# Performance work log

Hardware: AMD Instinct MI355X
Metric: run time of the kernel (lower is better)

The kernel has to match this reference:

```python
import jax, jax.numpy as jnp
import numpy as np

NFEATS = 768; NHIDS = 768; H = 8; HD = NHIDS // H
NT = 32768; NC = 32768; NS = 32768; DEG = 8; E = NT * DEG
ALPHA = 0.2  # LeakyReLU negative slope


def setup_inputs() -> dict:
    key = jax.random.key(0)
    ks = jax.random.split(key, 16)
    f32 = jnp.float32
    dst = jnp.repeat(jnp.arange(NT, dtype=jnp.int32), DEG)  # uniform in-degree mailbox
    return {
        'h': jax.random.normal(ks[0], (NT, NFEATS), f32),
        'hb_c_src': jax.random.normal(ks[1], (NC, NHIDS), f32),
        'hb_s_src': jax.random.normal(ks[2], (NS, NHIDS), f32),
        'Wg': jax.random.normal(ks[3], (H, NFEATS, HD), f32) * 0.05,
        'bg': jnp.zeros((H, HD), f32),
        'ag': jax.random.normal(ks[4], (H, 2 * HD), f32) * 0.1,
        'agb': jnp.zeros((H,), f32),
        'Wx': jax.random.normal(ks[5], (H, NHIDS, HD), f32) * 0.05,
        'bx': jnp.zeros((H, HD), f32),
        'ax': jax.random.normal(ks[6], (H, 2 * HD), f32) * 0.1,
        'axb': jnp.zeros((H,), f32),
        'Wih': jax.random.normal(ks[7], (3 * NHIDS, NHIDS), f32) * 0.02,
        'Whh': jax.random.normal(ks[8], (3 * NHIDS, NHIDS), f32) * 0.02,
        'bih': jnp.zeros((3 * NHIDS,), f32),
        'bhh': jnp.zeros((3 * NHIDS,), f32),
        'intra_src': jax.random.randint(ks[9], (E,), 0, NT, jnp.int32),
        'intra_dst': dst,
        'c_src': jax.random.randint(ks[10], (E,), 0, NC, jnp.int32),
        'c_dst': dst,
        's_src': jax.random.randint(ks[11], (E,), 0, NS, jnp.int32),
        's_dst': dst,
    }


def _attend(Wh_s, Wh_d, src, dst, a, ab, n_dst):
    """Multi-head GAT edge attention + segment softmax + weighted aggregation.
    Wh_s: [Ns,H,D] src projections, Wh_d: [Nd,H,D] dst projections.
    a([Wh_src||Wh_dst]) decomposed as a_src.Wh_src + a_dst.Wh_dst + bias."""
    D = Wh_s.shape[-1]
    e = (jnp.einsum('nhd,hd->nh', Wh_s, a[:, :D])[src]
         + jnp.einsum('nhd,hd->nh', Wh_d, a[:, D:])[dst] + ab)  # [E,H]
    e = jax.nn.leaky_relu(e, ALPHA)
    m = jax.ops.segment_max(e, dst, num_segments=n_dst)
    ex = jnp.exp(e - m[dst])
    den = jax.ops.segment_sum(ex, dst, num_segments=n_dst)
    att = ex / den[dst]  # per-dst softmax over incoming edges (DGL mailbox softmax)
    out = jax.ops.segment_sum(Wh_s[src] * att[..., None], dst, num_segments=n_dst)
    return out.reshape(n_dst, H * D)  # concat heads


def _forward(h, hb_c_src, hb_s_src, Wg, bg, ag, agb, Wx, bx, ax, axb,
             Wih, Whh, bih, bhh, intra_src, intra_dst, c_src, c_dst, s_src, s_dst):
    n = h.shape[0]
    # intra-turn GAT (x = self.gat(g, t)); dropout is identity in eval mode
    Wh = jnp.einsum('nf,hfd->nhd', h, Wg) + bg
    x = _attend(Wh, Wh, intra_src, intra_dst, ag, agb, n)
    # cross-turn inversed GAT; dst nodes' 'hb' feature is the fresh gat output x;
    # counter_bw and support_bw share the same xgat weights.
    Wx_d = jnp.einsum('nf,hfd->nhd', x, Wx) + bx
    Wc_s = jnp.einsum('nf,hfd->nhd', hb_c_src, Wx) + bx
    h_c = _attend(Wc_s, Wx_d, c_src, c_dst, ax, axb, n)
    Ws_s = jnp.einsum('nf,hfd->nhd', hb_s_src, Wx) + bx
    h_s = _attend(Ws_s, Wx_d, s_src, s_dst, ax, axb, n)
    hid = 0.5 * h_c + 0.5 * h_s
    # GRUCell(x, hid)
    gi = x @ Wih.T + bih
    gh = hid @ Whh.T + bhh
    ir, iz, inn = jnp.split(gi, 3, axis=1)
    hr, hz, hn = jnp.split(gh, 3, axis=1)
    r = jax.nn.sigmoid(ir + hr)
    z = jax.nn.sigmoid(iz + hz)
    cand = jnp.tanh(inn + r * hn)
    return (1.0 - z) * cand + z * hid


def reference(h, hb_c_src, hb_s_src, Wg, bg, ag, agb, Wx, bx, ax, axb,
              Wih, Whh, bih, bhh, intra_src, intra_dst, c_src, c_dst, s_src, s_dst):
    return _forward(h, hb_c_src, hb_s_src, Wg, bg, ag, agb, Wx, bx, ax, axb,
                    Wih, Whh, bih, bhh, intra_src, intra_dst, c_src, c_dst, s_src, s_dst)
```

## Files before the change

kernel.cpp:

```cpp
#include <hip/hip_runtime.h>
#include <hip/hip_bf16.h>
#include <math.h>

#define NT 32768
#define HD 96
#define DEG 8
#define NE (NT * DEG)
#define LRELU_ALPHA 0.2f
#define CH 16384

typedef __attribute__((ext_vector_type(8))) short bf16x8;
typedef __attribute__((ext_vector_type(8))) unsigned short u16x8;
typedef __attribute__((ext_vector_type(4))) unsigned short u16x4;
typedef __attribute__((ext_vector_type(4))) float f32x4;

__device__ __forceinline__ unsigned short f2bf(float x) {
    union { float f; unsigned u; } v; v.f = x;
    unsigned r = v.u + 0x7FFFu + ((v.u >> 16) & 1u);
    return (unsigned short)(r >> 16);
}
__device__ __forceinline__ float bf2f(unsigned short u) {
    union { unsigned u; float f; } v; v.u = ((unsigned)u) << 16; return v.f;
}

__device__ __forceinline__ void gload_lds16(const void* g, void* l) {
    __builtin_amdgcn_global_load_lds(
        (const __attribute__((address_space(1))) void*)g,
        (__attribute__((address_space(3))) void*)l, 16, 0, 0);
}


__global__ void packWT(const float* __restrict__ W, unsigned short* __restrict__ T) {
    int idx = blockIdx.x * 256 + threadIdx.x;
    if (idx >= 768 * 768) return;
    int c = idx / 768, f = idx % 768;
    T[idx] = f2bf(W[(size_t)(c / HD) * 768 * HD + (size_t)f * HD + (c % HD)]);
}

__global__ void cvt_bf8(const float* __restrict__ X, unsigned short* __restrict__ Y, int n8) {
    int i = blockIdx.x * 256 + threadIdx.x;
    if (i >= n8) return;
    float4 a = ((const float4*)X)[2 * i];
    float4 b = ((const float4*)X)[2 * i + 1];
    u16x8 p;
    p[0] = f2bf(a.x); p[1] = f2bf(a.y); p[2] = f2bf(a.z); p[3] = f2bf(a.w);
    p[4] = f2bf(b.x); p[5] = f2bf(b.y); p[6] = f2bf(b.z); p[7] = f2bf(b.w);
    ((u16x8*)Y)[i] = p;
}

__global__ void packWV(const float* __restrict__ Wx, const float* __restrict__ ax,
                       const float* __restrict__ bx,
                       float* __restrict__ wv, float* __restrict__ cd) {
    int idx = blockIdx.x * 256 + threadIdx.x;
    if (idx < 8 * 768) {
        int h = idx / 768, f = idx % 768;
        const float* wp = Wx + (size_t)h * 768 * HD + (size_t)f * HD;
        const float* ap = ax + h * 2 * HD + HD;
        float s = 0.f;
        for (int d = 0; d < HD; d++) s += wp[d] * ap[d];
        wv[idx] = s;
    }
    if (idx < 8) {
        const float* bp = bx + idx * HD;
        const float* ap = ax + idx * 2 * HD + HD;
        float s = 0.f;
        for (int d = 0; d < HD; d++) s += bp[d] * ap[d];
        cd[idx] = s;
    }
}

__global__ __launch_bounds__(256, 4) void mgemm3s(
    const float* __restrict__ A1, const float* __restrict__ A2,
    const float* __restrict__ A3,
    const unsigned short* __restrict__ BT1, const unsigned short* __restrict__ BT2,
    const float* __restrict__ bias1, const float* __restrict__ bias2,
    unsigned short* __restrict__ C1, unsigned short* __restrict__ C2,
    unsigned short* __restrict__ C3,
    int mt1, int mt2, int N, int K) {
    __shared__ unsigned short Alds[2][128 * 40];
    __shared__ unsigned short Blds[2][128 * 32];
    const int tid = threadIdx.x;
    const int w = tid >> 6, l = tid & 63;
    const int wr = w >> 1, wc = w & 1;
    const int lrow = l & 15, lk = l >> 4;

    const int nx = gridDim.x;
    const int nwg = nx * gridDim.y;
    int lin = blockIdx.y * nx + blockIdx.x;
    if ((nwg & 7) == 0) lin = (lin & 7) * (nwg >> 3) + (lin >> 3);
    int bm = lin / nx;
    const int bn = lin % nx;

    const int part = (bm >= mt1) + (bm >= mt2);
    const float* A           = part == 0 ? A1 : (part == 1 ? A2 : A3);
    const unsigned short* BT = part == 0 ? BT1 : BT2;
    const float* bias        = part == 0 ? bias1 : bias2;
    unsigned short* C        = part == 0 ? C1 : (part == 1 ? C2 : C3);
    bm -= (part == 1 ? mt1 : (part == 2 ? mt2 : 0));

    const unsigned short* bsrc[2];
    #pragma unroll
    for (int q = 0; q < 2; q++) {
        int idx = q * 256 + tid;
        int r = idx >> 2, s = idx & 3;
        int kw = s ^ ((r >> 1) & 3);
        bsrc[q] = BT + (size_t)(bn * 128 + r) * K + kw * 8;
    }
    const int ldst = (w * 64) * 8;

    const int arow = tid >> 1;
    const int as0 = (tid & 1) * 2;
    const float* aptr = A + (size_t)(bm * 128 + arow) * K + as0 * 8;

    auto stageA = [&](int buf, int k0) {
        float4 a0 = *(const float4*)(aptr + k0);
        float4 a1 = *(const float4*)(aptr + k0 + 4);
        float4 a2 = *(const float4*)(aptr + k0 + 8);
        float4 a3 = *(const float4*)(aptr + k0 + 12);
        u16x8 p0, p1;
        p0[0] = f2bf(a0.x); p0[1] = f2bf(a0.y); p0[2] = f2bf(a0.z); p0[3] = f2bf(a0.w);
        p0[4] = f2bf(a1.x); p0[5] = f2bf(a1.y); p0[6] = f2bf(a1.z); p0[7] = f2bf(a1.w);
        p1[0] = f2bf(a2.x); p1[1] = f2bf(a2.y); p1[2] = f2bf(a2.z); p1[3] = f2bf(a2.w);
        p1[4] = f2bf(a3.x); p1[5] = f2bf(a3.y); p1[6] = f2bf(a3.z); p1[7] = f2bf(a3.w);
        *(u16x8*)(&Alds[buf][arow * 40 + as0 * 8]) = p0;
        *(u16x8*)(&Alds[buf][arow * 40 + as0 * 8 + 8]) = p1;
    };

    gload_lds16(bsrc[0], &Blds[0][ldst]);
    gload_lds16(bsrc[1], &Blds[0][2048 + ldst]);
    stageA(0, 0);

    f32x4 acc[4][4] = {};
    const int nt = K >> 5;

    for (int t = 0; t < nt; ++t) {
        const int cur = t & 1;
        __syncthreads();
        if (t + 1 < nt) {
            const int k1 = (t + 1) << 5;
            gload_lds16(bsrc[0] + k1, &Blds[cur ^ 1][ldst]);
            gload_lds16(bsrc[1] + k1, &Blds[cur ^ 1][2048 + ldst]);
            stageA(cur ^ 1, k1);
        }
        bf16x8 af[4], bfv[4];
        #pragma unroll
        for (int i = 0; i < 4; i++) {
            int r = wr * 64 + i * 16 + lrow;
            af[i] = *(const bf16x8*)(&Alds[cur][r * 40 + lk * 8]);
        }
        #pragma unroll
        for (int j = 0; j < 4; j++) {
            int r = wc * 64 + j * 16 + lrow;
            int s = lk ^ ((r >> 1) & 3);
            bfv[j] = *(const bf16x8*)(&Blds[cur][r * 32 + s * 8]);
        }
        #pragma unroll
        for (int i = 0; i < 4; i++)
            #pragma unroll
            for (int j = 0; j < 4; j++)
                acc[i][j] = __builtin_amdgcn_mfma_f32_16x16x32_bf16(af[i], bfv[j], acc[i][j], 0, 0, 0);
    }

    const size_t crow0 = (size_t)bm * 128 + wr * 64;
    const int ccol0 = bn * 128 + wc * 64;
    #pragma unroll
    for (int j = 0; j < 4; j++) {
        int col = ccol0 + j * 16 + lrow;
        float bv = bias[col];
        #pragma unroll
        for (int i = 0; i < 4; i++) {
            size_t row = crow0 + i * 16 + lk * 4;
            #pragma unroll
            for (int e = 0; e < 4; e++)
                C[(row + e) * N + col] = f2bf(acc[i][j][e] + bv);
        }
    }
}

__global__ __launch_bounds__(256, 4) void mgemm2(
    const unsigned short* __restrict__ A1, const unsigned short* __restrict__ A2,
    const unsigned short* __restrict__ BT1, const unsigned short* __restrict__ BT2,
    const float* __restrict__ bias1, const float* __restrict__ bias2,
    unsigned short* __restrict__ C1, unsigned short* __restrict__ C2,
    int mt1, int N, int K) {
    __shared__ unsigned short Alds[2][128 * 32];
    __shared__ unsigned short Blds[2][128 * 32];
    const int tid = threadIdx.x;
    const int w = tid >> 6, l = tid & 63;
    const int wr = w >> 1, wc = w & 1;
    const int lrow = l & 15, lk = l >> 4;

    const int nx = gridDim.x;
    const int nwg = nx * gridDim.y;
    int lin = blockIdx.y * nx + blockIdx.x;
    if ((nwg & 7) == 0) lin = (lin & 7) * (nwg >> 3) + (lin >> 3);
    int bm = lin / nx;
    const int bn = lin % nx;

    const bool p1 = bm < mt1;
    const unsigned short* A  = p1 ? A1 : A2;
    const unsigned short* BT = p1 ? BT1 : BT2;
    const float* bias        = p1 ? bias1 : bias2;
    unsigned short* C        = p1 ? C1 : C2;
    if (!p1) bm -= mt1;

    const unsigned short* asrc[2];
    const unsigned short* bsrc[2];
    #pragma unroll
    for (int q = 0; q < 2; q++) {
        int idx = q * 256 + tid;
        int r = idx >> 2, s = idx & 3;
        int kw = s ^ ((r >> 1) & 3);
        asrc[q] = A  + (size_t)(bm * 128 + r) * K + kw * 8;
        bsrc[q] = BT + (size_t)(bn * 128 + r) * K + kw * 8;
    }
    const int ldst = (w * 64) * 8;

    gload_lds16(asrc[0], &Alds[0][ldst]);
    gload_lds16(asrc[1], &Alds[0][2048 + ldst]);
    gload_lds16(bsrc[0], &Blds[0][ldst]);
    gload_lds16(bsrc[1], &Blds[0][2048 + ldst]);

    f32x4 acc[4][4] = {};
    const int nt = K >> 5;

    for (int t = 0; t < nt; ++t) {
        const int cur = t & 1;
        __syncthreads();
        if (t + 1 < nt) {
            const int k1 = (t + 1) << 5;
            gload_lds16(asrc[0] + k1, &Alds[cur ^ 1][ldst]);
            gload_lds16(asrc[1] + k1, &Alds[cur ^ 1][2048 + ldst]);
            gload_lds16(bsrc[0] + k1, &Blds[cur ^ 1][ldst]);
            gload_lds16(bsrc[1] + k1, &Blds[cur ^ 1][2048 + ldst]);
        }
        bf16x8 af[4], bfv[4];
        #pragma unroll
        for (int i = 0; i < 4; i++) {
            int r = wr * 64 + i * 16 + lrow;
            int s = lk ^ ((r >> 1) & 3);
            af[i] = *(const bf16x8*)(&Alds[cur][r * 32 + s * 8]);
        }
        #pragma unroll
        for (int j = 0; j < 4; j++) {
            int r = wc * 64 + j * 16 + lrow;
            int s = lk ^ ((r >> 1) & 3);
            bfv[j] = *(const bf16x8*)(&Blds[cur][r * 32 + s * 8]);
        }
        #pragma unroll
        for (int i = 0; i < 4; i++)
            #pragma unroll
            for (int j = 0; j < 4; j++)
                acc[i][j] = __builtin_amdgcn_mfma_f32_16x16x32_bf16(af[i], bfv[j], acc[i][j], 0, 0, 0);
    }

    const size_t crow0 = (size_t)bm * 128 + wr * 64;
    const int ccol0 = bn * 128 + wc * 64;
    #pragma unroll
    for (int j = 0; j < 4; j++) {
        int col = ccol0 + j * 16 + lrow;
        float bv = bias[col];
        #pragma unroll
        for (int i = 0; i < 4; i++) {
            size_t row = crow0 + i * 16 + lk * 4;
            #pragma unroll
            for (int e = 0; e < 4; e++)
                C[(row + e) * N + col] = f2bf(acc[i][j][e] + bv);
        }
    }
}

__global__ __launch_bounds__(256) void escore2(
    const unsigned short* __restrict__ X, const float* __restrict__ a,
    float* __restrict__ s0out, float* __restrict__ s1out) {
    __shared__ float av0[768], av1[768];
    for (int t = threadIdx.x; t < 768; t += 256) {
        int hh = t / HD, d = t % HD;
        av0[t] = a[hh * 2 * HD + d];
        av1[t] = a[hh * 2 * HD + HD + d];
    }
    __syncthreads();
    int idx = blockIdx.x * 256 + threadIdx.x;
    int row = idx >> 3, hh = idx & 7;
    const unsigned short* xp = X + (size_t)row * 768 + hh * HD;
    const float* a0 = av0 + hh * HD;
    const float* a1 = av1 + hh * HD;
    float s0 = 0.f, s1 = 0.f;
    #pragma unroll
    for (int q = 0; q < 12; q++) {
        u16x8 v = *(const u16x8*)(xp + q * 8);
        #pragma unroll
        for (int e = 0; e < 8; e++) {
            float x = bf2f(v[e]);
            s0 += x * a0[q * 8 + e];
            s1 += x * a1[q * 8 + e];
        }
    }
    s0out[idx] = s0;
    s1out[idx] = s1;
}

__global__ __launch_bounds__(256) void escore(
    const unsigned short* __restrict__ X, const float* __restrict__ a,
    int half, float* __restrict__ sc) {
    __shared__ float av[768];
    for (int t = threadIdx.x; t < 768; t += 256) {
        int hh = t / HD, d = t % HD;
        av[t] = a[hh * 2 * HD + half * HD + d];
    }
    __syncthreads();
    int idx = blockIdx.x * 256 + threadIdx.x;
    int row = idx >> 3, hh = idx & 7;
    const unsigned short* xp = X + (size_t)row * 768 + hh * HD;
    const float* ap = av + hh * HD;
    float s = 0.f;
    #pragma unroll
    for (int q = 0; q < 12; q++) {
        u16x8 v = *(const u16x8*)(xp + q * 8);
        #pragma unroll
        for (int e = 0; e < 8; e++) s += bf2f(v[e]) * ap[q * 8 + e];
    }
    sc[idx] = s;
}

__global__ __launch_bounds__(256) void escore_fold(
    const unsigned short* __restrict__ X, const float* __restrict__ wv,
    const float* __restrict__ cd, float* __restrict__ ed) {
    __shared__ float wvs[8][8][97];
    __shared__ float cds[8];
    for (int i = threadIdx.x; i < 8 * 8 * 96; i += 256) {
        int j = i / (8 * 96); int r = i % (8 * 96); int h = r / 96; int t = r % 96;
        wvs[j][h][t] = wv[h * 768 + j * 96 + t];
    }
    if (threadIdx.x < 8) cds[threadIdx.x] = cd[threadIdx.x];
    __syncthreads();
    int idx = blockIdx.x * 256 + threadIdx.x;
    int n = idx >> 3, j = idx & 7;
    const unsigned short* xp = X + (size_t)n * 768 + j * 96;
    float p[8] = {};
    #pragma unroll
    for (int q = 0; q < 12; q++) {
        u16x8 v = *(const u16x8*)(xp + q * 8);
        #pragma unroll
        for (int e = 0; e < 8; e++) {
            float x = bf2f(v[e]);
            #pragma unroll
            for (int h = 0; h < 8; h++) p[h] += x * wvs[j][h][q * 8 + e];
        }
    }
    #pragma unroll
    for (int o = 1; o < 8; o <<= 1)
        #pragma unroll
        for (int h = 0; h < 8; h++) p[h] += __shfl_xor(p[h], o, 64);
    ed[(size_t)n * 8 + j] = p[j] + cds[j];
}

__global__ __launch_bounds__(256) void attend_agg(
    const unsigned short* __restrict__ Whs, const float* __restrict__ es,
    const float* __restrict__ ed, const float* __restrict__ ab,
    const int* __restrict__ src, const int* __restrict__ dst,
    unsigned short* __restrict__ out) {
    const int wv = threadIdx.x >> 6, l = threadIdx.x & 63;
    const int seg = blockIdx.x * 4 + wv;
    const int hh = l >> 3, j = l & 7;
    int sj = src[seg * 8 + j];
    int dnode = dst[seg * 8];
    float e = es[(size_t)sj * 8 + hh] + ed[(size_t)dnode * 8 + hh] + ab[hh];
    e = e > 0.f ? e : LRELU_ALPHA * e;
    float m = e;
    #pragma unroll
    for (int o = 1; o < 8; o <<= 1) m = fmaxf(m, __shfl_xor(m, o, 64));
    float ex = expf(e - m);
    float s = ex;
    #pragma unroll
    for (int o = 1; o < 8; o <<= 1) s += __shfl_xor(s, o, 64);
    float att = ex / s;

    #pragma unroll
    for (int u = 0; u < 3; u++) {
        int c = 4 * l + 256 * u;
        int h = c / HD;
        float acc0 = 0.f, acc1 = 0.f, acc2 = 0.f, acc3 = 0.f;
        #pragma unroll
        for (int j2 = 0; j2 < 8; j2++) {
            float a = __shfl(att, h * 8 + j2, 64);
            int sid = __shfl(sj, j2, 64);
            u16x4 v = *(const u16x4*)(Whs + (size_t)sid * 768 + c);
            acc0 += a * bf2f(v[0]); acc1 += a * bf2f(v[1]);
            acc2 += a * bf2f(v[2]); acc3 += a * bf2f(v[3]);
        }
        u16x4 r;
        r[0] = f2bf(acc0); r[1] = f2bf(acc1); r[2] = f2bf(acc2); r[3] = f2bf(acc3);
        *(u16x4*)(out + (size_t)dnode * 768 + c) = r;
    }
}

__global__ __launch_bounds__(256) void attend2(
    const unsigned short* __restrict__ Wc, const unsigned short* __restrict__ Ws,
    const float* __restrict__ esC, const float* __restrict__ esS,
    const float* __restrict__ ed, const float* __restrict__ ab,
    const int* __restrict__ csrc, const int* __restrict__ ssrc,
    const int* __restrict__ dst, unsigned short* __restrict__ outH) {
    const int wv = threadIdx.x >> 6, l = threadIdx.x & 63;
    const int seg = blockIdx.x * 4 + wv;
    const int hh = l >> 3, j = l & 7;
    int cj = csrc[seg * 8 + j];
    int sj = ssrc[seg * 8 + j];
    int dnode = dst[seg * 8];
    float edv = ed[(size_t)dnode * 8 + hh] + ab[hh];

    float eC = esC[(size_t)cj * 8 + hh] + edv;
    eC = eC > 0.f ? eC : LRELU_ALPHA * eC;
    float mC = eC;
    #pragma unroll
    for (int o = 1; o < 8; o <<= 1) mC = fmaxf(mC, __shfl_xor(mC, o, 64));
    float exC = expf(eC - mC);
    float sC = exC;
    #pragma unroll
    for (int o = 1; o < 8; o <<= 1) sC += __shfl_xor(sC, o, 64);
    float attC = exC / sC;

    float eS = esS[(size_t)sj * 8 + hh] + edv;
    eS = eS > 0.f ? eS : LRELU_ALPHA * eS;
    float mS = eS;
    #pragma unroll
    for (int o = 1; o < 8; o <<= 1) mS = fmaxf(mS, __shfl_xor(mS, o, 64));
    float exS = expf(eS - mS);
    float sS = exS;
    #pragma unroll
    for (int o = 1; o < 8; o <<= 1) sS += __shfl_xor(sS, o, 64);
    float attS = exS / sS;

    #pragma unroll
    for (int u = 0; u < 3; u++) {
        int c = 4 * l + 256 * u;
        int h = c / HD;
        float acc0 = 0.f, acc1 = 0.f, acc2 = 0.f, acc3 = 0.f;
        #pragma unroll
        for (int j2 = 0; j2 < 8; j2++) {
            float a = __shfl(attC, h * 8 + j2, 64);
            int sid = __shfl(cj, j2, 64);
            u16x4 v = *(const u16x4*)(Wc + (size_t)sid * 768 + c);
            acc0 += a * bf2f(v[0]); acc1 += a * bf2f(v[1]);
            acc2 += a * bf2f(v[2]); acc3 += a * bf2f(v[3]);
        }
        #pragma unroll
        for (int j2 = 0; j2 < 8; j2++) {
            float a = __shfl(attS, h * 8 + j2, 64);
            int sid = __shfl(sj, j2, 64);
            u16x4 v = *(const u16x4*)(Ws + (size_t)sid * 768 + c);
            acc0 += a * bf2f(v[0]); acc1 += a * bf2f(v[1]);
            acc2 += a * bf2f(v[2]); acc3 += a * bf2f(v[3]);
        }
        u16x4 r;
        r[0] = f2bf(0.5f * acc0); r[1] = f2bf(0.5f * acc1);
        r[2] = f2bf(0.5f * acc2); r[3] = f2bf(0.5f * acc3);
        *(u16x4*)(outH + (size_t)dnode * 768 + c) = r;
    }
}

__global__ __launch_bounds__(256) void gru_elem(
    const unsigned short* __restrict__ gi, const unsigned short* __restrict__ gh,
    const unsigned short* __restrict__ hid, float* __restrict__ out) {
    int idx = blockIdx.x * 256 + threadIdx.x;
    int nrow = idx / 96, c8 = (idx % 96) * 8;
    const unsigned short* gip = gi + (size_t)nrow * 2304 + c8;
    const unsigned short* ghp = gh + (size_t)nrow * 2304 + c8;
    u16x8 vir = *(const u16x8*)(gip);
    u16x8 viz = *(const u16x8*)(gip + 768);
    u16x8 vin = *(const u16x8*)(gip + 1536);
    u16x8 vhr = *(const u16x8*)(ghp);
    u16x8 vhz = *(const u16x8*)(ghp + 768);
    u16x8 vhn = *(const u16x8*)(ghp + 1536);
    u16x8 vh  = *(const u16x8*)(hid + (size_t)nrow * 768 + c8);
    float res[8];
    #pragma unroll
    for (int e = 0; e < 8; e++) {
        float r = 1.f / (1.f + expf(-(bf2f(vir[e]) + bf2f(vhr[e]))));
        float z = 1.f / (1.f + expf(-(bf2f(viz[e]) + bf2f(vhz[e]))));
        float cand = tanhf(bf2f(vin[e]) + r * bf2f(vhn[e]));
        res[e] = (1.f - z) * cand + z * bf2f(vh[e]);
    }
    float* op = out + (size_t)nrow * 768 + c8;
    *(float4*)(op)     = make_float4(res[0], res[1], res[2], res[3]);
    *(float4*)(op + 4) = make_float4(res[4], res[5], res[6], res[7]);
}

extern "C" void kernel_launch(void* const* d_in, const int* in_sizes, int n_in,
                              void* d_out, int out_size, void* d_ws, size_t ws_size,
                              hipStream_t stream) {
    const float* h    = (const float*)d_in[0];
    const float* hbc  = (const float*)d_in[1];
    const float* hbs  = (const float*)d_in[2];
    const float* Wg   = (const float*)d_in[3];
    const float* bg   = (const float*)d_in[4];
    const float* ag   = (const float*)d_in[5];
    const float* agb  = (const float*)d_in[6];
    const float* Wx   = (const float*)d_in[7];
    const float* bx   = (const float*)d_in[8];
    const float* ax   = (const float*)d_in[9];
    const float* axb  = (const float*)d_in[10];
    const float* Wih  = (const float*)d_in[11];
    const float* Whh  = (const float*)d_in[12];
    const float* bih  = (const float*)d_in[13];
    const float* bhh  = (const float*)d_in[14];
    const int* i_src  = (const int*)d_in[15];
    const int* i_dst  = (const int*)d_in[16];
    const int* c_src  = (const int*)d_in[17];
    const int* c_dst  = (const int*)d_in[18];
    const int* s_src  = (const int*)d_in[19];
    const int* s_dst  = (const int*)d_in[20];
    float* out = (float*)d_out;

    const size_t SZ = (size_t)NT * 768;
    unsigned short* Xb   = (unsigned short*)d_ws;
    unsigned short* Hdb  = Xb + SZ;
    unsigned short* GIb  = Hdb + SZ;
    unsigned short* GHb  = GIb + (size_t)CH * 2304;
    unsigned short* W2gT = GHb + (size_t)CH * 2304;
    unsigned short* W2xT = W2gT + 768 * 768;
    unsigned short* WihB = W2xT + 768 * 768;
    unsigned short* WhhB = WihB + 2304 * 768;
    float* EScat = (float*)(WhhB + 2304 * 768);
    float* ED    = EScat + 2 * NE;
    float* ESI   = ED + NE;
    float* EDI   = ESI + NE;
    float* WV    = EDI + NE;
    float* CD    = WV + 8 * 768;
    unsigned short* Pcat = (unsigned short*)d_out;

    dim3 blk(256);
    packWT<<<(768 * 768 + 255) / 256, blk, 0, stream>>>(Wg, W2gT);
    packWT<<<(768 * 768 + 255) / 256, blk, 0, stream>>>(Wx, W2xT);
    cvt_bf8<<<(2304 * 768 / 8 + 255) / 256, blk, 0, stream>>>(Wih, WihB, 2304 * 768 / 8);
    cvt_bf8<<<(2304 * 768 / 8 + 255) / 256, blk, 0, stream>>>(Whh, WhhB, 2304 * 768 / 8);
    packWV<<<(8 * 768 + 255) / 256, blk, 0, stream>>>(Wx, ax, bx, WV, CD);

    dim3 gproj(6, 768);
    mgemm3s<<<gproj, blk, 0, stream>>>(h, hbc, hbs, W2gT, W2xT, bg, bx,
                                       Hdb, Pcat, Pcat + SZ, 256, 512, 768, 768);
    escore2<<<NE / 256, blk, 0, stream>>>(Hdb, ag, ESI, EDI);
    attend_agg<<<NT / 4, blk, 0, stream>>>(Hdb, ESI, EDI, agb, i_src, i_dst, Xb);
    escore_fold<<<NE / 256, blk, 0, stream>>>(Xb, WV, CD, ED);
    escore<<<2 * NE / 256, blk, 0, stream>>>(Pcat, ax, 0, EScat);
    attend2<<<NT / 4, blk, 0, stream>>>(Pcat, Pcat + SZ, EScat, EScat + NE, ED, axb,
                                        c_src, s_src, c_dst, Hdb);
    dim3 ggru(18, 256);
    for (int c0 = 0; c0 < NT; c0 += CH) {
        mgemm2<<<ggru, blk, 0, stream>>>(Xb + (size_t)c0 * 768, Hdb + (size_t)c0 * 768,
                                         WihB, WhhB, bih, bhh, GIb, GHb,
                                         128, 2304, 768);
        gru_elem<<<(CH * 96) / 256, blk, 0, stream>>>(GIb, GHb, Hdb + (size_t)c0 * 768, out + (size_t)c0 * 768);
    }
}
```

Before: 903.2 us.

## Fuse attention score dot products into projection GEMM epilogue and aggregation kernel

Removes the separate escore2, escore and escore_fold kernels. The projection GEMM epilogue now computes the per-head src/dst attention scores from the fp32 accumulators and accumulates them with atomicAdd into zeroed buffers. The attend_agg kernel computes the folded dst score from its aggregated output before rounding to bf16. This avoids re-reading three 32768x768 bf16 tensors. In exchange it adds memsets, atomics and shuffle reductions in the GEMM epilogue, and scores are now computed from unrounded values, so results can differ slightly.

New measurement: 993.0 us. 1.1x slower.

```diff
diff --git a/kernel.cpp b/kernel.cpp
--- a/kernel.cpp
+++ b/kernel.cpp
@@ -48,9 +48,9 @@
     ((u16x8*)Y)[i] = p;
 }
 
-__global__ void packWV(const float* __restrict__ Wx, const float* __restrict__ ax,
-                       const float* __restrict__ bx,
-                       float* __restrict__ wv, float* __restrict__ cd) {
+__global__ void packWVT(const float* __restrict__ Wx, const float* __restrict__ ax,
+                        const float* __restrict__ bx,
+                        float* __restrict__ wvT, float* __restrict__ cd) {
     int idx = blockIdx.x * 256 + threadIdx.x;
     if (idx < 8 * 768) {
         int h = idx / 768, f = idx % 768;
@@ -58,7 +58,7 @@
         const float* ap = ax + h * 2 * HD + HD;
         float s = 0.f;
         for (int d = 0; d < HD; d++) s += wp[d] * ap[d];
-        wv[idx] = s;
+        wvT[(size_t)f * 8 + h] = s;
     }
     if (idx < 8) {
         const float* bp = bx + idx * HD;
@@ -67,6 +67,17 @@
         for (int d = 0; d < HD; d++) s += bp[d] * ap[d];
         cd[idx] = s;
     }
+}
+
+__global__ void avpack(const float* __restrict__ ag, const float* __restrict__ ax,
+                       float* __restrict__ av0g, float* __restrict__ av1g,
+                       float* __restrict__ axsg) {
+    int c = blockIdx.x * 256 + threadIdx.x;
+    if (c >= 768) return;
+    int h = c / HD, d = c % HD;
+    av0g[c] = ag[h * 2 * HD + d];
+    av1g[c] = ag[h * 2 * HD + HD + d];
+    axsg[c] = ax[h * 2 * HD + d];
 }
 
 __global__ __launch_bounds__(256, 4) void mgemm3s(
@@ -76,6 +87,10 @@
     const float* __restrict__ bias1, const float* __restrict__ bias2,
     unsigned short* __restrict__ C1, unsigned short* __restrict__ C2,
     unsigned short* __restrict__ C3,
+    const float* __restrict__ aq0_0, const float* __restrict__ aq1_0,
+    const float* __restrict__ aq_12,
+    float* __restrict__ s0_0, float* __restrict__ s1_0,
+    float* __restrict__ s_1, float* __restrict__ s_2,
     int mt1, int mt2, int N, int K) {
     __shared__ unsigned short Alds[2][128 * 40];
     __shared__ unsigned short Blds[2][128 * 32];
@@ -96,6 +111,10 @@
     const unsigned short* BT = part == 0 ? BT1 : BT2;
     const float* bias        = part == 0 ? bias1 : bias2;
     unsigned short* C        = part == 0 ? C1 : (part == 1 ? C2 : C3);
+    const float* aq0 = part == 0 ? aq0_0 : aq_12;
+    const float* aq1 = part == 0 ? aq1_0 : (const float*)0;
+    float* S0 = part == 0 ? s0_0 : (part == 1 ? s_1 : s_2);
+    float* S1 = part == 0 ? s1_0 : (float*)0;
     bm -= (part == 1 ? mt1 : (part == 2 ? mt2 : 0));
 
     const unsigned short* bsrc[2];
@@ -163,16 +182,64 @@
 
     const size_t crow0 = (size_t)bm * 128 + wr * 64;
     const int ccol0 = bn * 128 + wc * 64;
+    const int hbase = ccol0 / 96;
+    const int colB = (hbase + 1) * 96;
+
+    float bvj[4], wa0[4], wa1[4];
+    int hiJ[4];
     #pragma unroll
     for (int j = 0; j < 4; j++) {
         int col = ccol0 + j * 16 + lrow;
-        float bv = bias[col];
+        bvj[j] = bias[col];
+        wa0[j] = aq0[col];
+        wa1[j] = S1 ? aq1[col] : 0.f;
+        hiJ[j] = col >= colB;
+    }
+
+    #pragma unroll
+    for (int j = 0; j < 4; j++) {
+        int col = ccol0 + j * 16 + lrow;
         #pragma unroll
         for (int i = 0; i < 4; i++) {
             size_t row = crow0 + i * 16 + lk * 4;
             #pragma unroll
             for (int e = 0; e < 4; e++)
-                C[(row + e) * N + col] = f2bf(acc[i][j][e] + bv);
+                C[(row + e) * N + col] = f2bf(acc[i][j][e] + bvj[j]);
+        }
+    }
+
+    #pragma unroll
+    for (int i = 0; i < 4; i++) {
+        #pragma unroll
+        for (int e = 0; e < 4; e++) {
+            float p0 = 0.f, p1 = 0.f, q0 = 0.f, q1 = 0.f;
+            #pragma unroll
+            for (int j = 0; j < 4; j++) {
+                float v = acc[i][j][e] + bvj[j];
+                float m = v * wa0[j];
+                p0 += hiJ[j] ? 0.f : m;
+                p1 += hiJ[j] ? m : 0.f;
+                if (S1) {
+                    float m2 = v * wa1[j];
+                    q0 += hiJ[j] ? 0.f : m2;
+                    q1 += hiJ[j] ? m2 : 0.f;
+                }
+            }
+            #pragma unroll
+            for (int o = 1; o < 16; o <<= 1) {
+                p0 += __shfl_xor(p0, o, 64);
+                p1 += __shfl_xor(p1, o, 64);
+                if (S1) { q0 += __shfl_xor(q0, o, 64); q1 += __shfl_xor(q1, o, 64); }
+            }
+            if (lrow == 0) {
+                size_t r = crow0 + i * 16 + lk * 4 + e;
+                atomicAdd(&S0[r * 8 + hbase], p0);
+                if (hbase < 7) atomicAdd(&S0[r * 8 + hbase + 1], p1);
+                if (S1) {
+                    atomicAdd(&S1[r * 8 + hbase], q0);
+                    if (hbase < 7) atomicAdd(&S1[r * 8 + hbase + 1], q1);
+                }
+            }
         }
     }
 }
@@ -270,96 +337,13 @@
     }
 }
 
-__global__ __launch_bounds__(256) void escore2(
-    const unsigned short* __restrict__ X, const float* __restrict__ a,
-    float* __restrict__ s0out, float* __restrict__ s1out) {
-    __shared__ float av0[768], av1[768];
-    for (int t = threadIdx.x; t < 768; t += 256) {
-        int hh = t / HD, d = t % HD;
-        av0[t] = a[hh * 2 * HD + d];
-        av1[t] = a[hh * 2 * HD + HD + d];
-    }
-    __syncthreads();
-    int idx = blockIdx.x * 256 + threadIdx.x;
-    int row = idx >> 3, hh = idx & 7;
-    const unsigned short* xp = X + (size_t)row * 768 + hh * HD;
-    const float* a0 = av0 + hh * HD;
-    const float* a1 = av1 + hh * HD;
-    float s0 = 0.f, s1 = 0.f;
-    #pragma unroll
-    for (int q = 0; q < 12; q++) {
-        u16x8 v = *(const u16x8*)(xp + q * 8);
-        #pragma unroll
-        for (int e = 0; e < 8; e++) {
-            float x = bf2f(v[e]);
-            s0 += x * a0[q * 8 + e];
-            s1 += x * a1[q * 8 + e];
-        }
-    }
-    s0out[idx] = s0;
-    s1out[idx] = s1;
-}
-
-__global__ __launch_bounds__(256) void escore(
-    const unsigned short* __restrict__ X, const float* __restrict__ a,
-    int half, float* __restrict__ sc) {
-    __shared__ float av[768];
-    for (int t = threadIdx.x; t < 768; t += 256) {
-        int hh = t / HD, d = t % HD;
-        av[t] = a[hh * 2 * HD + half * HD + d];
-    }
-    __syncthreads();
-    int idx = blockIdx.x * 256 + threadIdx.x;
-    int row = idx >> 3, hh = idx & 7;
-    const unsigned short* xp = X + (size_t)row * 768 + hh * HD;
-    const float* ap = av + hh * HD;
-    float s = 0.f;
-    #pragma unroll
-    for (int q = 0; q < 12; q++) {
-        u16x8 v = *(const u16x8*)(xp + q * 8);
-        #pragma unroll
-        for (int e = 0; e < 8; e++) s += bf2f(v[e]) * ap[q * 8 + e];
-    }
-    sc[idx] = s;
-}
-
-__global__ __launch_bounds__(256) void escore_fold(
-    const unsigned short* __restrict__ X, const float* __restrict__ wv,
-    const float* __restrict__ cd, float* __restrict__ ed) {
-    __shared__ float wvs[8][8][97];
-    __shared__ float cds[8];
-    for (int i = threadIdx.x; i < 8 * 8 * 96; i += 256) {
-        int j = i / (8 * 96); int r = i % (8 * 96); int h = r / 96; int t = r % 96;
-        wvs[j][h][t] = wv[h * 768 + j * 96 + t];
-    }
-    if (threadIdx.x < 8) cds[threadIdx.x] = cd[threadIdx.x];
-    __syncthreads();
-    int idx = blockIdx.x * 256 + threadIdx.x;
-    int n = idx >> 3, j = idx & 7;
-    const unsigned short* xp = X + (size_t)n * 768 + j * 96;
-    float p[8] = {};
-    #pragma unroll
-    for (int q = 0; q < 12; q++) {
-        u16x8 v = *(const u16x8*)(xp + q * 8);
-        #pragma unroll
-        for (int e = 0; e < 8; e++) {
-            float x = bf2f(v[e]);
-            #pragma unroll
-            for (int h = 0; h < 8; h++) p[h] += x * wvs[j][h][q * 8 + e];
-        }
-    }
-    #pragma unroll
-    for (int o = 1; o < 8; o <<= 1)
-        #pragma unroll
-        for (int h = 0; h < 8; h++) p[h] += __shfl_xor(p[h], o, 64);
-    ed[(size_t)n * 8 + j] = p[j] + cds[j];
-}
-
 __global__ __launch_bounds__(256) void attend_agg(
     const unsigned short* __restrict__ Whs, const float* __restrict__ es,
     const float* __restrict__ ed, const float* __restrict__ ab,
     const int* __restrict__ src, const int* __restrict__ dst,
-    unsigned short* __restrict__ out) {
+    unsigned short* __restrict__ out,
+    const float* __restrict__ wvT, const float* __restrict__ cd,
+    float* __restrict__ edout) {
     const int wv = threadIdx.x >> 6, l = threadIdx.x & 63;
     const int seg = blockIdx.x * 4 + wv;
     const int hh = l >> 3, j = l & 7;
@@ -376,6 +360,7 @@
     for (int o = 1; o < 8; o <<= 1) s += __shfl_xor(s, o, 64);
     float att = ex / s;
 
+    float p8[8] = {};
     #pragma unroll
     for (int u = 0; u < 3; u++) {
         int c = 4 * l + 256 * u;
@@ -392,6 +377,29 @@
         u16x4 r;
         r[0] = f2bf(acc0); r[1] = f2bf(acc1); r[2] = f2bf(acc2); r[3] = f2bf(acc3);
         *(u16x4*)(out + (size_t)dnode * 768 + c) = r;
+        float xs[4] = {acc0, acc1, acc2, acc3};
+        #pragma unroll
+        for (int jj = 0; jj < 4; jj++) {
+            const float* wp = wvT + (size_t)(c + jj) * 8;
+            float4 w0 = *(const float4*)wp;
+            float4 w1 = *(const float4*)(wp + 4);
+            p8[0] += xs[jj] * w0.x; p8[1] += xs[jj] * w0.y;
+            p8[2] += xs[jj] * w0.z; p8[3] += xs[jj] * w0.w;
+            p8[4] += xs[jj] * w1.x; p8[5] += xs[jj] * w1.y;
+            p8[6] += xs[jj] * w1.z; p8[7] += xs[jj] * w1.w;
+        }
+    }
+    #pragma unroll
+    for (int o = 1; o < 64; o <<= 1) {
+        #pragma unroll
+        for (int k = 0; k < 8; k++) p8[k] += __shfl_xor(p8[k], o, 64);
+    }
+    if (l == 0) {
+        float4 c0 = *(const float4*)cd;
+        float4 c1 = *(const float4*)(cd + 4);
+        float* op = edout + (size_t)dnode * 8;
+        *(float4*)op       = make_float4(p8[0] + c0.x, p8[1] + c0.y, p8[2] + c0.z, p8[3] + c0.w);
+        *(float4*)(op + 4) = make_float4(p8[4] + c1.x, p8[5] + c1.y, p8[6] + c1.z, p8[7] + c1.w);
     }
 }
 
@@ -525,24 +533,32 @@
     float* ED    = EScat + 2 * NE;
     float* ESI   = ED + NE;
     float* EDI   = ESI + NE;
-    float* WV    = EDI + NE;
-    float* CD    = WV + 8 * 768;
+    float* WVT   = EDI + NE;
+    float* CD    = WVT + 768 * 8;
+    float* AV0   = CD + 8;
+    float* AV1   = AV0 + 768;
+    float* AXS   = AV1 + 768;
     unsigned short* Pcat = (unsigned short*)d_out;
 
     dim3 blk(256);
+    hipMemsetAsync(EScat, 0, (size_t)2 * NE * sizeof(float), stream);
+    hipMemsetAsync(ESI,   0, (size_t)2 * NE * sizeof(float), stream);
+
     packWT<<<(768 * 768 + 255) / 256, blk, 0, stream>>>(Wg, W2gT);
     packWT<<<(768 * 768 + 255) / 256, blk, 0, stream>>>(Wx, W2xT);
     cvt_bf8<<<(2304 * 768 / 8 + 255) / 256, blk, 0, stream>>>(Wih, WihB, 2304 * 768 / 8);
     cvt_bf8<<<(2304 * 768 / 8 + 255) / 256, blk, 0, stream>>>(Whh, WhhB, 2304 * 768 / 8);
-    packWV<<<(8 * 768 + 255) / 256, blk, 0, stream>>>(Wx, ax, bx, WV, CD);
+    packWVT<<<(8 * 768 + 255) / 256, blk, 0, stream>>>(Wx, ax, bx, WVT, CD);
+    avpack<<<3, blk, 0, stream>>>(ag, ax, AV0, AV1, AXS);
 
     dim3 gproj(6, 768);
     mgemm3s<<<gproj, blk, 0, stream>>>(h, hbc, hbs, W2gT, W2xT, bg, bx,
-                                       Hdb, Pcat, Pcat + SZ, 256, 512, 768, 768);
-    escore2<<<NE / 256, blk, 0, stream>>>(Hdb, ag, ESI, EDI);
-    attend_agg<<<NT / 4, blk, 0, stream>>>(Hdb, ESI, EDI, agb, i_src, i_dst, Xb);
-    escore_fold<<<NE / 256, blk, 0, stream>>>(Xb, WV, CD, ED);
-    escore<<<2 * NE / 256, blk, 0, stream>>>(Pcat, ax, 0, EScat);
+                                       Hdb, Pcat, Pcat + SZ,
+                                       AV0, AV1, AXS,
+                                       ESI, EDI, EScat, EScat + NE,
+                                       256, 512, 768, 768);
+    attend_agg<<<NT / 4, blk, 0, stream>>>(Hdb, ESI, EDI, agb, i_src, i_dst, Xb,
+                                           WVT, CD, ED);
     attend2<<<NT / 4, blk, 0, stream>>>(Pcat, Pcat + SZ, EScat, EScat + NE, ED, axb,
                                         c_src, s_src, c_dst, Hdb);
     dim3 ggru(18, 256);
```
